# Optimization experiments

Measured on AMD Instinct MI355X. Metric: run time of the kernel, lower is better.

The kernel has to match this reference:

```python
import jax, jax.numpy as jnp
import numpy as np

NK_DIM = 64
EK_DIM = 16
TEMPERATURE = 8.0
NEG_INF = -1e9


def setup_inputs() -> dict:
    key = jax.random.key(0)
    k1, k2, k3, k4, k5 = jax.random.split(key, 5)
    B, H, N, DV = 4, 8, 256, 64
    q = jax.random.normal(k1, (B, H, N, NK_DIM + EK_DIM), dtype=jnp.float32)
    nk = jax.random.normal(k2, (B, H, N, NK_DIM), dtype=jnp.float32)
    ek = jax.random.normal(k3, (B, H, N, N, EK_DIM), dtype=jnp.float32)
    v = jax.random.normal(k4, (B, H, N, DV), dtype=jnp.float32)
    mask = jax.random.randint(k5, (B, 1, N, N), 0, 2, dtype=jnp.int32)
    return {"q": q, "nk": nk, "ek": ek, "v": v, "mask": mask}


def reference(q, nk, ek, v, mask):
    # split query into node part and edge part
    qn = q[..., :NK_DIM]   # [B,H,N,nk]
    qe = q[..., NK_DIM:]   # [B,H,N,ek]
    # standard scaled dot-product term: [B,H,N,N]
    node_attn = jnp.einsum('bhqd,bhkd->bhqk', qn, nk)
    # per-edge key term: contract qe against 5D edge keys -> [B,H,N,N]
    edge_attn = jnp.einsum('bhqd,bhqkd->bhqk', qe, ek)
    attn = (node_attn + edge_attn) / TEMPERATURE
    attn = jnp.where(mask == 0, jnp.asarray(NEG_INF, attn.dtype), attn)
    attn = jax.nn.softmax(attn, axis=-1)
    # dropout p=0.0 (identity) in this reference
    output = jnp.einsum('bhqk,bhkd->bhqd', attn, v)
    return output, attn
```

## Files before the change

kernel.cpp:

```cpp
#include <hip/hip_runtime.h>

constexpr int NKD = 64;
constexpr int EKD = 16;
constexpr int QD  = 80;
constexpr int NN  = 256;
constexpr int DVD = 64;
constexpr int BB  = 4;
constexpr int HH  = 8;
constexpr int QT  = 8;
constexpr int NT  = 256;

__global__ __launch_bounds__(256, 4) void sdpe_kernel(
    const float* __restrict__ q, const float* __restrict__ nk,
    const float* __restrict__ ek, const float* __restrict__ v,
    const int* __restrict__ mask, float* __restrict__ out, float* __restrict__ attn_out)
{
    const int bid  = blockIdx.x;
    const int bh   = bid >> 5;
    const int q0   = (bid & 31) * QT;
    const int b    = bh >> 3;
    const int tid  = threadIdx.x;
    const int wave = tid >> 6;
    const int lane = tid & 63;

    __shared__ float s_q[QT * QD];
    __shared__ float s_S[QT * NN];
    __shared__ float s_nk[64 * 64];

    {
        const float4* src = (const float4*)(q + ((size_t)bh * NN + q0) * QD);
        if (tid < QT * QD / 4) ((float4*)s_q)[tid] = src[tid];
    }
    __syncthreads();

    {
        const int jb = tid & 3;
        const int kb = tid >> 2;
        const float4* ekb = (const float4*)ek + ((size_t)bh * NN + q0) * (NN * EKD / 4);
        #pragma unroll 2
        for (int r = 0; r < QT; ++r) {
            const float4 qe4 = *(const float4*)&s_q[r * QD + NKD + jb * 4];
            const float4 e0 = ekb[(size_t)r * 1024 + tid];
            const float4 e1 = ekb[(size_t)r * 1024 + tid + 256];
            const float4 e2 = ekb[(size_t)r * 1024 + tid + 512];
            const float4 e3 = ekb[(size_t)r * 1024 + tid + 768];
            float p0 = e0.x*qe4.x + e0.y*qe4.y + e0.z*qe4.z + e0.w*qe4.w;
            float p1 = e1.x*qe4.x + e1.y*qe4.y + e1.z*qe4.z + e1.w*qe4.w;
            float p2 = e2.x*qe4.x + e2.y*qe4.y + e2.z*qe4.z + e2.w*qe4.w;
            float p3 = e3.x*qe4.x + e3.y*qe4.y + e3.z*qe4.z + e3.w*qe4.w;
            p0 += __shfl_xor(p0, 1);  p0 += __shfl_xor(p0, 2);
            p1 += __shfl_xor(p1, 1);  p1 += __shfl_xor(p1, 2);
            p2 += __shfl_xor(p2, 1);  p2 += __shfl_xor(p2, 2);
            p3 += __shfl_xor(p3, 1);  p3 += __shfl_xor(p3, 2);
            const float pw = (jb == 0) ? p0 : (jb == 1) ? p1 : (jb == 2) ? p2 : p3;
            s_S[r * NN + kb + 64 * jb] = pw;
        }
    }
    __syncthreads();

    for (int kt = 0; kt < 4; ++kt) {
        {
            const float4* src = (const float4*)nk + ((size_t)bh * NN + kt * 64) * (NKD / 4);
            #pragma unroll
            for (int i = 0; i < 4; ++i) {
                const int f   = tid + 256 * i;
                const int row = f >> 4, c4 = f & 15;
                *(float4*)&s_nk[row * 64 + ((c4 ^ (row & 7)) << 2)] = src[f];
            }
        }
        __syncthreads();
        float acc0 = 0.f, acc1 = 0.f;
        #pragma unroll
        for (int j4 = 0; j4 < 16; ++j4) {
            const float4 n4 = *(const float4*)&s_nk[lane * 64 + ((j4 ^ (lane & 7)) << 2)];
            const float4 qa = *(const float4*)&s_q[wave * QD + j4 * 4];
            const float4 qb = *(const float4*)&s_q[(wave + 4) * QD + j4 * 4];
            acc0 += n4.x*qa.x + n4.y*qa.y + n4.z*qa.z + n4.w*qa.w;
            acc1 += n4.x*qb.x + n4.y*qb.y + n4.z*qb.z + n4.w*qb.w;
        }
        const int kg = kt * 64 + lane;
        s_S[wave * NN + kg]       += acc0;
        s_S[(wave + 4) * NN + kg] += acc1;
        __syncthreads();
    }

    #pragma unroll
    for (int rr = 0; rr < 2; ++rr) {
        const int r = wave + rr * 4;
        const size_t rowg = (size_t)bh * NN + q0 + r;
        float4 f = *(const float4*)&s_S[r * NN + lane * 4];
        const int4 m4 = *(const int4*)(mask + ((size_t)b * NN + q0 + r) * NN + lane * 4);
        f.x = (m4.x == 0) ? -1e9f : f.x * 0.125f;
        f.y = (m4.y == 0) ? -1e9f : f.y * 0.125f;
        f.z = (m4.z == 0) ? -1e9f : f.z * 0.125f;
        f.w = (m4.w == 0) ? -1e9f : f.w * 0.125f;
        float mx = fmaxf(fmaxf(f.x, f.y), fmaxf(f.z, f.w));
        #pragma unroll
        for (int o = 32; o >= 1; o >>= 1) mx = fmaxf(mx, __shfl_xor(mx, o));
        float4 e;
        e.x = __expf(f.x - mx); e.y = __expf(f.y - mx);
        e.z = __expf(f.z - mx); e.w = __expf(f.w - mx);
        float s = e.x + e.y + e.z + e.w;
        #pragma unroll
        for (int o = 32; o >= 1; o >>= 1) s += __shfl_xor(s, o);
        const float inv = 1.f / s;
        e.x *= inv; e.y *= inv; e.z *= inv; e.w *= inv;
        *(float4*)&s_S[r * NN + lane * 4] = e;
        *(float4*)(attn_out + rowg * NN + lane * 4) = e;
    }
    __syncthreads();

    {
        const int d4 = lane & 15;
        const int kq = lane >> 4;
        float4 a0 = make_float4(0.f,0.f,0.f,0.f), a1 = make_float4(0.f,0.f,0.f,0.f);
        const float* vb = v + (size_t)bh * NN * DVD + d4 * 4;
        #pragma unroll 4
        for (int i = 0; i < 16; ++i) {
            const int k0 = i * 16 + kq * 4;
            const float4 w0 = *(const float4*)&s_S[wave * NN + k0];
            const float4 w1 = *(const float4*)&s_S[(wave + 4) * NN + k0];
            const float4 v0 = *(const float4*)(vb + (size_t)(k0 + 0) * DVD);
            const float4 v1 = *(const float4*)(vb + (size_t)(k0 + 1) * DVD);
            const float4 v2 = *(const float4*)(vb + (size_t)(k0 + 2) * DVD);
            const float4 v3 = *(const float4*)(vb + (size_t)(k0 + 3) * DVD);
            a0.x += w0.x*v0.x + w0.y*v1.x + w0.z*v2.x + w0.w*v3.x;
            a0.y += w0.x*v0.y + w0.y*v1.y + w0.z*v2.y + w0.w*v3.y;
            a0.z += w0.x*v0.z + w0.y*v1.z + w0.z*v2.z + w0.w*v3.z;
            a0.w += w0.x*v0.w + w0.y*v1.w + w0.z*v2.w + w0.w*v3.w;
            a1.x += w1.x*v0.x + w1.y*v1.x + w1.z*v2.x + w1.w*v3.x;
            a1.y += w1.x*v0.y + w1.y*v1.y + w1.z*v2.y + w1.w*v3.y;
            a1.z += w1.x*v0.z + w1.y*v1.z + w1.z*v2.z + w1.w*v3.z;
            a1.w += w1.x*v0.w + w1.y*v1.w + w1.z*v2.w + w1.w*v3.w;
        }
        a0.x += __shfl_xor(a0.x, 16); a0.y += __shfl_xor(a0.y, 16);
        a0.z += __shfl_xor(a0.z, 16); a0.w += __shfl_xor(a0.w, 16);
        a1.x += __shfl_xor(a1.x, 16); a1.y += __shfl_xor(a1.y, 16);
        a1.z += __shfl_xor(a1.z, 16); a1.w += __shfl_xor(a1.w, 16);
        a0.x += __shfl_xor(a0.x, 32); a0.y += __shfl_xor(a0.y, 32);
        a0.z += __shfl_xor(a0.z, 32); a0.w += __shfl_xor(a0.w, 32);
        a1.x += __shfl_xor(a1.x, 32); a1.y += __shfl_xor(a1.y, 32);
        a1.z += __shfl_xor(a1.z, 32); a1.w += __shfl_xor(a1.w, 32);
        if (kq == 0) {
            const size_t rowg0 = (size_t)bh * NN + q0 + wave;
            *(float4*)(out + rowg0 * DVD + d4 * 4)       = a0;
            *(float4*)(out + (rowg0 + 4) * DVD + d4 * 4) = a1;
        }
    }
}

extern "C" void kernel_launch(void* const* d_in, const int* in_sizes, int n_in,
                              void* d_out, int out_size, void* d_ws, size_t ws_size,
                              hipStream_t stream) {
    const float* q    = (const float*)d_in[0];
    const float* nk   = (const float*)d_in[1];
    const float* ek   = (const float*)d_in[2];
    const float* v    = (const float*)d_in[3];
    const int*   mask = (const int*)d_in[4];

    float* out      = (float*)d_out;
    float* attn_out = out + (size_t)BB * HH * NN * DVD;

    const int nblocks = BB * HH * (NN / QT);
    sdpe_kernel<<<nblocks, NT, 0, stream>>>(q, nk, ek, v, mask, out, attn_out);
}
```

Before: 220.9 us.

## Split node-score GEMM into separate kernel and repartition PV by key across waves

Moves the q·nk dot products, scaling and masking into a first kernel that writes pre-masked scores into the attn output buffer, with each thread holding one nk row in registers and 32 queries per block. This removes the four rounds of per-block nk staging in shared memory that were repeated for every 8-query tile. The main kernel reads those scores back, adds the edge term and runs softmax in place. Its PV stage now splits the keys across waves, each wave accumulating all 8 rows, and combines the partials through shared memory, so each V row is read once per block instead of once per wave. The cost is an extra launch and a round trip of the score matrix through global memory, plus more accumulator registers.

```diff
diff --git a/kernel.cpp b/kernel.cpp
--- a/kernel.cpp
+++ b/kernel.cpp
@@ -8,28 +8,77 @@
 constexpr int BB  = 4;
 constexpr int HH  = 8;
 constexpr int QT  = 8;
-constexpr int NT  = 256;
+constexpr int K1QT = 32;
 
-__global__ __launch_bounds__(256, 4) void sdpe_kernel(
+__global__ __launch_bounds__(256) void node_score_kernel(
     const float* __restrict__ q, const float* __restrict__ nk,
+    const int* __restrict__ mask, float* __restrict__ s0)
+{
+    const int bid = blockIdx.x;
+    const int bh  = bid >> 3;
+    const int q0  = (bid & 7) * K1QT;
+    const int b   = bh >> 3;
+    const int tid = threadIdx.x;
+
+    __shared__ float4 s_qn[K1QT * 16];
+
+    {
+        const float4* qsrc = (const float4*)(q + ((size_t)bh * NN + q0) * QD);
+        #pragma unroll
+        for (int i = tid; i < K1QT * 16; i += 256) {
+            const int r = i >> 4, j = i & 15;
+            s_qn[i] = qsrc[r * 20 + j];
+        }
+    }
+    float4 nkr[16];
+    {
+        const float4* nkp = (const float4*)(nk + ((size_t)bh * NN + tid) * NKD);
+        #pragma unroll
+        for (int j = 0; j < 16; ++j) nkr[j] = nkp[j];
+    }
+    __syncthreads();
+
+    float*     dst  = s0   + ((size_t)bh * NN + q0) * NN + tid;
+    const int* mrow = mask + ((size_t)b  * NN + q0) * NN + tid;
+    #pragma unroll 4
+    for (int r = 0; r < K1QT; ++r) {
+        float acc = 0.f;
+        #pragma unroll
+        for (int j = 0; j < 16; ++j) {
+            const float4 a = s_qn[r * 16 + j], n = nkr[j];
+            acc += a.x * n.x + a.y * n.y + a.z * n.z + a.w * n.w;
+        }
+        acc *= 0.125f;
+        if (mrow[(size_t)r * NN] == 0) acc = -1.0e9f;
+        dst[(size_t)r * NN] = acc;
+    }
+}
+
+__global__ __launch_bounds__(256) void sdpe_kernel(
+    const float* __restrict__ q, const float* __restrict__ s0,
     const float* __restrict__ ek, const float* __restrict__ v,
-    const int* __restrict__ mask, float* __restrict__ out, float* __restrict__ attn_out)
+    float* __restrict__ out, float* __restrict__ attn_out)
 {
     const int bid  = blockIdx.x;
     const int bh   = bid >> 5;
     const int q0   = (bid & 31) * QT;
-    const int b    = bh >> 3;
     const int tid  = threadIdx.x;
     const int wave = tid >> 6;
     const int lane = tid & 63;
 
-    __shared__ float s_q[QT * QD];
-    __shared__ float s_S[QT * NN];
-    __shared__ float s_nk[64 * 64];
+    __shared__ float  s_S[QT * NN];
+    __shared__ float4 s_qe[QT * 4];
+    __shared__ float4 s_part[4][QT][16];
 
     {
-        const float4* src = (const float4*)(q + ((size_t)bh * NN + q0) * QD);
-        if (tid < QT * QD / 4) ((float4*)s_q)[tid] = src[tid];
+        const float4* ssrc = (const float4*)(s0 + ((size_t)bh * NN + q0) * NN);
+        float4* sdst = (float4*)s_S;
+        sdst[tid]       = ssrc[tid];
+        sdst[tid + 256] = ssrc[tid + 256];
+        if (tid < QT * 4) {
+            const int r = tid >> 2, j = tid & 3;
+            s_qe[tid] = *(const float4*)(q + ((size_t)bh * NN + q0 + r) * QD + NKD + j * 4);
+        }
     }
     __syncthreads();
 
@@ -39,7 +88,7 @@
         const float4* ekb = (const float4*)ek + ((size_t)bh * NN + q0) * (NN * EKD / 4);
         #pragma unroll 2
         for (int r = 0; r < QT; ++r) {
-            const float4 qe4 = *(const float4*)&s_q[r * QD + NKD + jb * 4];
+            const float4 qe4 = s_qe[r * 4 + jb];
             const float4 e0 = ekb[(size_t)r * 1024 + tid];
             const float4 e1 = ekb[(size_t)r * 1024 + tid + 256];
             const float4 e2 = ekb[(size_t)r * 1024 + tid + 512];
@@ -53,47 +102,16 @@
             p2 += __shfl_xor(p2, 1);  p2 += __shfl_xor(p2, 2);
             p3 += __shfl_xor(p3, 1);  p3 += __shfl_xor(p3, 2);
             const float pw = (jb == 0) ? p0 : (jb == 1) ? p1 : (jb == 2) ? p2 : p3;
-            s_S[r * NN + kb + 64 * jb] = pw;
+            s_S[r * NN + kb + 64 * jb] += 0.125f * pw;
         }
     }
     __syncthreads();
-
-    for (int kt = 0; kt < 4; ++kt) {
-        {
-            const float4* src = (const float4*)nk + ((size_t)bh * NN + kt * 64) * (NKD / 4);
-            #pragma unroll
-            for (int i = 0; i < 4; ++i) {
-                const int f   = tid + 256 * i;
-                const int row = f >> 4, c4 = f & 15;
-                *(float4*)&s_nk[row * 64 + ((c4 ^ (row & 7)) << 2)] = src[f];
-            }
-        }
-        __syncthreads();
-        float acc0 = 0.f, acc1 = 0.f;
-        #pragma unroll
-        for (int j4 = 0; j4 < 16; ++j4) {
-            const float4 n4 = *(const float4*)&s_nk[lane * 64 + ((j4 ^ (lane & 7)) << 2)];
-            const float4 qa = *(const float4*)&s_q[wave * QD + j4 * 4];
-            const float4 qb = *(const float4*)&s_q[(wave + 4) * QD + j4 * 4];
-            acc0 += n4.x*qa.x + n4.y*qa.y + n4.z*qa.z + n4.w*qa.w;
-            acc1 += n4.x*qb.x + n4.y*qb.y + n4.z*qb.z + n4.w*qb.w;
-        }
-        const int kg = kt * 64 + lane;
-        s_S[wave * NN + kg]       += acc0;
-        s_S[(wave + 4) * NN + kg] += acc1;
-        __syncthreads();
-    }
 
     #pragma unroll
     for (int rr = 0; rr < 2; ++rr) {
         const int r = wave + rr * 4;
         const size_t rowg = (size_t)bh * NN + q0 + r;
         float4 f = *(const float4*)&s_S[r * NN + lane * 4];
-        const int4 m4 = *(const int4*)(mask + ((size_t)b * NN + q0 + r) * NN + lane * 4);
-        f.x = (m4.x == 0) ? -1e9f : f.x * 0.125f;
-        f.y = (m4.y == 0) ? -1e9f : f.y * 0.125f;
-        f.z = (m4.z == 0) ? -1e9f : f.z * 0.125f;
-        f.w = (m4.w == 0) ? -1e9f : f.w * 0.125f;
         float mx = fmaxf(fmaxf(f.x, f.y), fmaxf(f.z, f.w));
         #pragma unroll
         for (int o = 32; o >= 1; o >>= 1) mx = fmaxf(mx, __shfl_xor(mx, o));
@@ -113,39 +131,49 @@
     {
         const int d4 = lane & 15;
         const int kq = lane >> 4;
-        float4 a0 = make_float4(0.f,0.f,0.f,0.f), a1 = make_float4(0.f,0.f,0.f,0.f);
+        float4 acc[QT];
+        #pragma unroll
+        for (int r = 0; r < QT; ++r) acc[r] = make_float4(0.f, 0.f, 0.f, 0.f);
+
         const float* vb = v + (size_t)bh * NN * DVD + d4 * 4;
-        #pragma unroll 4
-        for (int i = 0; i < 16; ++i) {
-            const int k0 = i * 16 + kq * 4;
-            const float4 w0 = *(const float4*)&s_S[wave * NN + k0];
-            const float4 w1 = *(const float4*)&s_S[(wave + 4) * NN + k0];
+        #pragma unroll
+        for (int i = 0; i < 4; ++i) {
+            const int k0 = wave * 64 + i * 16 + kq * 4;
             const float4 v0 = *(const float4*)(vb + (size_t)(k0 + 0) * DVD);
             const float4 v1 = *(const float4*)(vb + (size_t)(k0 + 1) * DVD);
             const float4 v2 = *(const float4*)(vb + (size_t)(k0 + 2) * DVD);
             const float4 v3 = *(const float4*)(vb + (size_t)(k0 + 3) * DVD);
-            a0.x += w0.x*v0.x + w0.y*v1.x + w0.z*v2.x + w0.w*v3.x;
-            a0.y += w0.x*v0.y + w0.y*v1.y + w0.z*v2.y + w0.w*v3.y;
-            a0.z += w0.x*v0.z + w0.y*v1.z + w0.z*v2.z + w0.w*v3.z;
-            a0.w += w0.x*v0.w + w0.y*v1.w + w0.z*v2.w + w0.w*v3.w;
-            a1.x += w1.x*v0.x + w1.y*v1.x + w1.z*v2.x + w1.w*v3.x;
-            a1.y += w1.x*v0.y + w1.y*v1.y + w1.z*v2.y + w1.w*v3.y;
-            a1.z += w1.x*v0.z + w1.y*v1.z + w1.z*v2.z + w1.w*v3.z;
-            a1.w += w1.x*v0.w + w1.y*v1.w + w1.z*v2.w + w1.w*v3.w;
+            #pragma unroll
+            for (int r = 0; r < QT; ++r) {
+                const float4 a4 = *(const float4*)&s_S[r * NN + k0];
+                acc[r].x += a4.x*v0.x + a4.y*v1.x + a4.z*v2.x + a4.w*v3.x;
+                acc[r].y += a4.x*v0.y + a4.y*v1.y + a4.z*v2.y + a4.w*v3.y;
+                acc[r].z += a4.x*v0.z + a4.y*v1.z + a4.z*v2.z + a4.w*v3.z;
+                acc[r].w += a4.x*v0.w + a4.y*v1.w + a4.z*v2.w + a4.w*v3.w;
+            }
         }
-        a0.x += __shfl_xor(a0.x, 16); a0.y += __shfl_xor(a0.y, 16);
-        a0.z += __shfl_xor(a0.z, 16); a0.w += __shfl_xor(a0.w, 16);
-        a1.x += __shfl_xor(a1.x, 16); a1.y += __shfl_xor(a1.y, 16);
-        a1.z += __shfl_xor(a1.z, 16); a1.w += __shfl_xor(a1.w, 16);
-        a0.x += __shfl_xor(a0.x, 32); a0.y += __shfl_xor(a0.y, 32);
-        a0.z += __shfl_xor(a0.z, 32); a0.w += __shfl_xor(a0.w, 32);
-        a1.x += __shfl_xor(a1.x, 32); a1.y += __shfl_xor(a1.y, 32);
-        a1.z += __shfl_xor(a1.z, 32); a1.w += __shfl_xor(a1.w, 32);
-        if (kq == 0) {
-            const size_t rowg0 = (size_t)bh * NN + q0 + wave;
-            *(float4*)(out + rowg0 * DVD + d4 * 4)       = a0;
-            *(float4*)(out + (rowg0 + 4) * DVD + d4 * 4) = a1;
+        #pragma unroll
+        for (int r = 0; r < QT; ++r) {
+            acc[r].x += __shfl_xor(acc[r].x, 16); acc[r].y += __shfl_xor(acc[r].y, 16);
+            acc[r].z += __shfl_xor(acc[r].z, 16); acc[r].w += __shfl_xor(acc[r].w, 16);
+            acc[r].x += __shfl_xor(acc[r].x, 32); acc[r].y += __shfl_xor(acc[r].y, 32);
+            acc[r].z += __shfl_xor(acc[r].z, 32); acc[r].w += __shfl_xor(acc[r].w, 32);
+            if (kq == 0) s_part[wave][r][d4] = acc[r];
         }
+    }
+    __syncthreads();
+
+    if (tid < QT * 16) {
+        const int r = tid >> 4, d4 = tid & 15;
+        const float4 p0 = s_part[0][r][d4], p1 = s_part[1][r][d4];
+        const float4 p2 = s_part[2][r][d4], p3 = s_part[3][r][d4];
+        float4 o;
+        o.x = p0.x + p1.x + p2.x + p3.x;
+        o.y = p0.y + p1.y + p2.y + p3.y;
+        o.z = p0.z + p1.z + p2.z + p3.z;
+        o.w = p0.w + p1.w + p2.w + p3.w;
+        const size_t rowg = (size_t)bh * NN + q0 + r;
+        *(float4*)(out + rowg * DVD + d4 * 4) = o;
     }
 }
 
@@ -161,6 +189,6 @@
     float* out      = (float*)d_out;
     float* attn_out = out + (size_t)BB * HH * NN * DVD;
 
-    const int nblocks = BB * HH * (NN / QT);
-    sdpe_kernel<<<nblocks, NT, 0, stream>>>(q, nk, ek, v, mask, out, attn_out);
+    node_score_kernel<<<BB * HH * (NN / K1QT), 256, 0, stream>>>(q, nk, mask, attn_out);
+    sdpe_kernel<<<BB * HH * (NN / QT), 256, 0, stream>>>(q, attn_out, ek, v, out, attn_out);
 }
```

Measured after the change: 235.5 us. +6.6%, slower.
